# Optimization experiments

Hardware: AMD Instinct MI355X
Metric: run time of the kernel (lower is better)

The kernel has to match this reference:

```python
import jax, jax.numpy as jnp
import numpy as np
from jax import lax

B, C_IN, C_OUT, H, W = 32, 96, 96, 56, 56
E = 8          # num_experts
HID = 576      # round(96 * 6)
K = 3          # depthwise kernel size


def setup_inputs() -> dict:
    key = jax.random.key(0)
    ks = jax.random.split(key, 12)
    f = lambda k, s, sc=0.05: jax.random.normal(k, s, dtype=jnp.float32) * sc
    return {
        "x": jax.random.normal(ks[0], (B, C_IN, H, W), dtype=jnp.float32),
        # router for expand conv (input = x, C_IN channels)
        "w_r1": f(ks[1], (E, C_IN)), "b_r1": jnp.zeros((E,), jnp.float32),
        # expert bank for 1x1 expand: [E, HID, C_IN]
        "w1": f(ks[2], (E, HID, C_IN)),
        "g1": jnp.ones((HID,), jnp.float32), "bt1": jnp.zeros((HID,), jnp.float32),
        "m1": f(ks[3], (HID,), 0.01), "v1": jax.random.uniform(ks[4], (HID,), dtype=jnp.float32) + 0.5,
        # router for depthwise conv (input = expanded features, HID channels)
        "w_r2": f(ks[5], (E, HID)), "b_r2": jnp.zeros((E,), jnp.float32),
        # expert bank for depthwise 3x3: [E, HID, K, K] (in/groups = 1)
        "w2": f(ks[6], (E, HID, K, K)),
        "g2": jnp.ones((HID,), jnp.float32), "bt2": jnp.zeros((HID,), jnp.float32),
        "m2": f(ks[7], (HID,), 0.01), "v2": jax.random.uniform(ks[8], (HID,), dtype=jnp.float32) + 0.5,
        # expert bank for 1x1 project: [E, C_OUT, HID]
        "w3": f(ks[9], (E, C_OUT, HID)),
        "g3": jnp.ones((C_OUT,), jnp.float32), "bt3": jnp.zeros((C_OUT,), jnp.float32),
        "m3": f(ks[10], (C_OUT,), 0.01), "v3": jax.random.uniform(ks[11], (C_OUT,), dtype=jnp.float32) + 0.5,
        # block-level router (input = x, C_IN channels) gating the project conv
        "w_r3": f(jax.random.fold_in(key, 99), (E, C_IN)), "b_r3": jnp.zeros((E,), jnp.float32),
    }


def _route(feat, Wf, bf):
    # BasicRouter: global avg pool -> Linear -> sigmoid. feat: [B, C, H, W] -> [B, E]
    return jax.nn.sigmoid(feat.mean(axis=(2, 3)) @ Wf.T + bf)


def _bn(y, g, b, m, v, eps=1e-5):
    inv = g * lax.rsqrt(v + eps)
    return y * inv[None, :, None, None] + (b - m * inv)[None, :, None, None]


def reference(x, w_r1, b_r1, w1, g1, bt1, m1, v1,
              w_r2, b_r2, w2, g2, bt2, m2, v2,
              w3, g3, bt3, m3, v3, w_r3, b_r3):
    r1 = _route(x, w_r1, b_r1)      # [B, E] gate for expand conv
    r_blk = _route(x, w_r3, b_r3)   # [B, E] block router gates project conv

    # --- CondConv 1x1 expand: per-sample mixed kernel as batched GEMM ---
    w1c = jnp.einsum('be,eoc->boc', r1, w1)              # [B, HID, C_IN]
    y = jnp.einsum('bchw,boc->bohw', x, w1c)             # [B, HID, H, W]
    y = jnp.clip(_bn(y, g1, bt1, m1, v1), 0.0, 6.0)      # ReLU6

    # --- CondConv depthwise 3x3 (groups = HID), router on expanded feats ---
    r2 = _route(y, w_r2, b_r2)                           # [B, E]
    kw = jnp.einsum('be,eckl->bckl', r2, w2).reshape(B * HID, 1, K, K)
    y = lax.conv_general_dilated(
        y.reshape(1, B * HID, H, W), kw, (1, 1), 'SAME',
        dimension_numbers=('NCHW', 'OIHW', 'NCHW'),
        feature_group_count=B * HID).reshape(B, HID, H, W)
    y = jnp.clip(_bn(y, g2, bt2, m2, v2), 0.0, 6.0)

    # --- CondConv 1x1 project, gated by the block router(x) ---
    w3c = jnp.einsum('be,eoc->boc', r_blk, w3)           # [B, C_OUT, HID]
    y = jnp.einsum('bchw,boc->bohw', y, w3c)             # [B, C_OUT, H, W]
    y = _bn(y, g3, bt3, m3, v3)

    return x + y  # stride==1 and inp==oup -> residual connection
```

## Files before the change

### kernel.cpp

```cpp
#include <hip/hip_runtime.h>
#include <hip/hip_bf16.h>

#define B_   32
#define CIN  96
#define COUT 96
#define NP   3136
#define NE   8
#define HIDD 576

typedef short bf16x8 __attribute__((ext_vector_type(8)));
typedef float f32x4 __attribute__((ext_vector_type(4)));

__device__ __forceinline__ unsigned short f2bf(float f) {
  __hip_bfloat16 h = __float2bfloat16(f);
  unsigned short u; __builtin_memcpy(&u, &h, 2); return u;
}
__device__ __forceinline__ float bf2f(unsigned short u) {
  unsigned int v = ((unsigned int)u) << 16;
  float f; __builtin_memcpy(&f, &v, 4); return f;
}
__device__ __forceinline__ float u2f(unsigned int v) {
  float f; __builtin_memcpy(&f, &v, 4); return f;
}

__global__ __launch_bounds__(256) void k_transpose(const float* __restrict__ x,
                                                   unsigned short* __restrict__ xt,
                                                   float* __restrict__ xmean) {
  __shared__ float tile[CIN][65];
  int bi = blockIdx.x; int b = bi / 49, pt = bi % 49; int p0 = pt * 64;
  int t = threadIdx.x;
  for (int j = t; j < CIN * 64; j += 256) {
    int c = j >> 6, pi = j & 63;
    tile[c][pi] = x[((size_t)(b * CIN + c)) * NP + p0 + pi];
  }
  __syncthreads();
  if (t < CIN) {
    float s = 0.f;
    for (int i = 0; i < 64; ++i) s += tile[t][i];
    atomicAdd(xmean + b * CIN + t, s);
  }
  for (int j = t; j < 64 * CIN; j += 256) {
    int p = j / CIN, c = j % CIN;
    xt[((size_t)(b * NP + p0 + p)) * CIN + c] = f2bf(tile[c][p]);
  }
}

__global__ __launch_bounds__(64) void k_router1(const float* __restrict__ xmean,
    const float* __restrict__ wr1, const float* __restrict__ br1,
    const float* __restrict__ wr3, const float* __restrict__ br3,
    float* __restrict__ r1, float* __restrict__ rblk) {
  int bi = blockIdx.x; int lane = threadIdx.x;
  const float* wr; const float* br; float* dst; int id;
  if (bi < 256) { wr = wr1; br = br1; dst = r1;   id = bi; }
  else          { wr = wr3; br = br3; dst = rblk; id = bi - 256; }
  int b = id >> 3, e = id & 7;
  float s = 0.f;
  for (int c = lane; c < CIN; c += 64)
    s += xmean[b * CIN + c] * (1.0f / NP) * wr[e * CIN + c];
  s += __shfl_xor(s, 1);  s += __shfl_xor(s, 2);  s += __shfl_xor(s, 4);
  s += __shfl_xor(s, 8);  s += __shfl_xor(s, 16); s += __shfl_xor(s, 32);
  if (lane == 0) dst[id] = 1.0f / (1.0f + __expf(-(s + br[e])));
}

__global__ __launch_bounds__(256) void k_bnprep(
    const float* g1, const float* bt1, const float* m1, const float* v1,
    const float* g2, const float* bt2, const float* m2, const float* v2,
    const float* g3, const float* bt3, const float* m3, const float* v3,
    float* sc1, float* bi1, float* sc2, float* bi2, float* sc3, float* bi3) {
  int i = blockIdx.x * 256 + threadIdx.x;
  if (i < HIDD) {
    float s = g1[i] * rsqrtf(v1[i] + 1e-5f); sc1[i] = s; bi1[i] = bt1[i] - m1[i] * s;
  } else if (i < 2 * HIDD) {
    int c = i - HIDD;
    float s = g2[c] * rsqrtf(v2[c] + 1e-5f); sc2[c] = s; bi2[c] = bt2[c] - m2[c] * s;
  } else if (i < 2 * HIDD + COUT) {
    int c = i - 2 * HIDD;
    float s = g3[c] * rsqrtf(v3[c] + 1e-5f); sc3[c] = s; bi3[c] = bt3[c] - m3[c] * s;
  }
}

__global__ __launch_bounds__(256) void k_mixw(
    const float* __restrict__ w1, const float* __restrict__ r1, unsigned short* __restrict__ w1c,
    const float* __restrict__ w3, const float* __restrict__ rblk, unsigned short* __restrict__ w3c) {
  __shared__ float rsh[256];
  int bi = blockIdx.x; int t = threadIdx.x;
  const float* w; const float* r; unsigned short* dst; int oc0;
  if (bi < 216) { w = w1; r = r1;   dst = w1c; oc0 = bi * 256; }
  else          { w = w3; r = rblk; dst = w3c; oc0 = (bi - 216) * 256; }
  rsh[t] = r[t];
  __syncthreads();
  int oc = oc0 + t;
  float wv[NE];
#pragma unroll
  for (int e = 0; e < NE; ++e) wv[e] = w[(size_t)e * 55296 + oc];
  for (int b = 0; b < B_; ++b) {
    float a = 0.f;
#pragma unroll
    for (int e = 0; e < NE; ++e) a += rsh[b * 8 + e] * wv[e];
    dst[(size_t)b * 55296 + oc] = f2bf(a);
  }
}

__global__ __launch_bounds__(256) void k_expand2(const unsigned short* __restrict__ xt,
    const unsigned short* __restrict__ w1c, const float* __restrict__ sc1,
    const float* __restrict__ bi1, unsigned short* __restrict__ y2,
    float* __restrict__ ysum) {
  __shared__ unsigned short As[64 * 104];
  __shared__ unsigned short Bs[64 * 104];
  int t = threadIdx.x;
  int p0 = blockIdx.x * 64, o0 = blockIdx.y * 64, b = blockIdx.z;
  const unsigned short* ag = w1c + (size_t)b * 55296 + (size_t)o0 * 96;
  const unsigned short* bg = xt + ((size_t)b * NP + p0) * 96;
  for (int j = t; j < 768; j += 256) {
    int r = j / 12, ch = j % 12;
    *(int4*)(As + r * 104 + ch * 8) = *(const int4*)(ag + r * 96 + ch * 8);
    *(int4*)(Bs + r * 104 + ch * 8) = *(const int4*)(bg + r * 96 + ch * 8);
  }
  __syncthreads();
  int lane = t & 63, wv = t >> 6;
  int m = lane & 15, q = lane >> 4;
  f32x4 acc[4];
#pragma unroll
  for (int nt = 0; nt < 4; ++nt) acc[nt] = 0.f;
#pragma unroll
  for (int kk = 0; kk < 3; ++kk) {
    bf16x8 af = *(const bf16x8*)(As + (wv * 16 + m) * 104 + kk * 32 + q * 8);
#pragma unroll
    for (int nt = 0; nt < 4; ++nt) {
      bf16x8 bfb = *(const bf16x8*)(Bs + (nt * 16 + m) * 104 + kk * 32 + q * 8);
      acc[nt] = __builtin_amdgcn_mfma_f32_16x16x32_bf16(af, bfb, acc[nt], 0, 0, 0);
    }
  }
  __syncthreads();
  float sc[4], bb[4];
#pragma unroll
  for (int i = 0; i < 4; ++i) {
    int o = o0 + wv * 16 + q * 4 + i;
    sc[i] = sc1[o]; bb[i] = bi1[o];
  }
  float rs[4] = {0.f, 0.f, 0.f, 0.f};
  unsigned short* T = As;
#pragma unroll
  for (int nt = 0; nt < 4; ++nt) {
    unsigned short pk[4];
#pragma unroll
    for (int i = 0; i < 4; ++i) {
      float v = acc[nt][i] * sc[i] + bb[i];
      v = fminf(fmaxf(v, 0.f), 6.f);
      rs[i] += v;
      pk[i] = f2bf(v);
    }
    uint2 pv; __builtin_memcpy(&pv, pk, 8);
    *(uint2*)(T + (nt * 16 + m) * 72 + wv * 16 + q * 4) = pv;
  }
#pragma unroll
  for (int i = 0; i < 4; ++i) {
    float r = rs[i];
    r += __shfl_xor(r, 1); r += __shfl_xor(r, 2);
    r += __shfl_xor(r, 4); r += __shfl_xor(r, 8);
    if (m == 0) atomicAdd(ysum + b * HIDD + o0 + wv * 16 + q * 4 + i, r);
  }
  __syncthreads();
  for (int j = t; j < 512; j += 256) {
    int r = j >> 3, ch = j & 7;
    *(int4*)(y2 + ((size_t)(b * NP + p0 + r)) * 576 + o0 + ch * 8) =
        *(const int4*)(T + r * 72 + ch * 8);
  }
}

__global__ __launch_bounds__(64) void k_router2(const float* __restrict__ ysum,
    const float* __restrict__ wr2, const float* __restrict__ br2, float* __restrict__ r2) {
  int id = blockIdx.x; int lane = threadIdx.x;
  int b = id >> 3, e = id & 7;
  float s = 0.f;
  for (int h = lane; h < HIDD; h += 64)
    s += ysum[b * HIDD + h] * (1.0f / NP) * wr2[e * HIDD + h];
  s += __shfl_xor(s, 1);  s += __shfl_xor(s, 2);  s += __shfl_xor(s, 4);
  s += __shfl_xor(s, 8);  s += __shfl_xor(s, 16); s += __shfl_xor(s, 32);
  if (lane == 0) r2[id] = 1.0f / (1.0f + __expf(-(s + br2[e])));
}

__global__ __launch_bounds__(256) void k_kwmix2(const float* __restrict__ r2,
    const float* __restrict__ w2, const float* __restrict__ sc2,
    const float* __restrict__ bi2, float* __restrict__ kwt) {
  int i = blockIdx.x * 256 + threadIdx.x;
  if (i >= B_ * HIDD) return;
  int b = i / HIDD, c = i - b * HIDD;
  float rr[NE];
#pragma unroll
  for (int e = 0; e < NE; ++e) rr[e] = r2[b * 8 + e];
  float sc = sc2[c];
  float* dst = kwt + (size_t)b * 5760 + c;
#pragma unroll
  for (int k = 0; k < 9; ++k) {
    float s = 0.f;
#pragma unroll
    for (int e = 0; e < NE; ++e) s += rr[e] * w2[((size_t)e * HIDD + c) * 9 + k];
    dst[k * 576] = s * sc;
  }
  dst[9 * 576] = bi2[c];
}

__device__ __forceinline__ f32x4 cvt4(uint2 v) {
  f32x4 r;
  r[0] = u2f(v.x << 16); r[1] = u2f(v.x & 0xffff0000u);
  r[2] = u2f(v.y << 16); r[3] = u2f(v.y & 0xffff0000u);
  return r;
}
__device__ __forceinline__ uint2 pack4(f32x4 v) {
  uint2 r;
  r.x = (unsigned)f2bf(v[0]) | ((unsigned)f2bf(v[1]) << 16);
  r.y = (unsigned)f2bf(v[2]) | ((unsigned)f2bf(v[3]) << 16);
  return r;
}
__device__ __forceinline__ f32x4 clamp6(f32x4 v) {
#pragma unroll
  for (int i = 0; i < 4; ++i) v[i] = fminf(fmaxf(v[i], 0.f), 6.f);
  return v;
}

__global__ __launch_bounds__(256) void k_dwise4(const unsigned short* __restrict__ y2,
    const float* __restrict__ kwt, unsigned short* __restrict__ z2) {
  int id = blockIdx.x * 256 + threadIdx.x;
  if (id >= 28 * 144 * 32) return;
  int cg = id % 144; int rest = id / 144;
  int hp = rest % 28; int b = rest / 28;
  int c = cg * 4, h0 = hp * 2;
  const float* kp = kwt + (size_t)b * 5760 + c;
  f32x4 tk[9], tb;
#pragma unroll
  for (int k = 0; k < 9; ++k) tk[k] = *(const f32x4*)(kp + k * 576);
  tb = *(const f32x4*)(kp + 9 * 576);
  bool ok0 = (hp > 0), ok3 = (hp < 27);
  int r0 = ok0 ? (h0 - 1) : h0;
  int r3 = ok3 ? (h0 + 2) : (h0 + 1);
  const unsigned short* rowp[4];
  rowp[0] = y2 + ((size_t)(b * NP + r0 * 56)) * 576 + c;
  rowp[1] = y2 + ((size_t)(b * NP + h0 * 56)) * 576 + c;
  rowp[2] = y2 + ((size_t)(b * NP + (h0 + 1) * 56)) * 576 + c;
  rowp[3] = y2 + ((size_t)(b * NP + r3 * 56)) * 576 + c;
  bool rok[4] = {ok0, true, true, ok3};
  unsigned short* zr0 = z2 + ((size_t)(b * NP + h0 * 56)) * 576 + c;
  unsigned short* zr1 = zr0 + (size_t)56 * 576;

  f32x4 P[4], C[4], N[4];
#pragma unroll
  for (int j = 0; j < 4; ++j) P[j] = 0.f;

#define LOADCOL(D, col) do {                                           \
    _Pragma("unroll") for (int j = 0; j < 4; ++j) {                    \
      uint2 raw; raw.x = 0u; raw.y = 0u;                               \
      if ((col) < 56 && rok[j]) raw = *(const uint2*)(rowp[j] + (size_t)(col) * 576); \
      D[j] = cvt4(raw);                                                \
    } } while (0)

#define DSTEP(PP, CC, NN, wcur) do {                                   \
    f32x4 o0 = tb, o1 = tb;                                            \
    _Pragma("unroll") for (int jj = 0; jj < 3; ++jj) {                 \
      o0 += PP[jj] * tk[jj * 3] + CC[jj] * tk[jj * 3 + 1] + NN[jj] * tk[jj * 3 + 2]; \
      o1 += PP[jj + 1] * tk[jj * 3] + CC[jj + 1] * tk[jj * 3 + 1] + NN[jj + 1] * tk[jj * 3 + 2]; \
    }                                                                  \
    *(uint2*)(zr0 + (size_t)(wcur) * 576) = pack4(clamp6(o0));         \
    *(uint2*)(zr1 + (size_t)(wcur) * 576) = pack4(clamp6(o1));         \
    LOADCOL(PP, (wcur) + 2);                                           \
  } while (0)

  LOADCOL(C, 0);
  LOADCOL(N, 1);
  for (int w = 0; w < 54; w += 3) {
    DSTEP(P, C, N, w);
    DSTEP(C, N, P, w + 1);
    DSTEP(N, P, C, w + 2);
  }
  DSTEP(P, C, N, 54);
  DSTEP(C, N, P, 55);
#undef DSTEP
#undef LOADCOL
}

__global__ __launch_bounds__(384) void k_project4(const unsigned short* __restrict__ z2,
    const unsigned short* __restrict__ w3c, const float* __restrict__ sc3,
    const float* __restrict__ bi3, const float* __restrict__ x, float* __restrict__ out) {
  __shared__ unsigned short As[96 * 72];
  __shared__ unsigned short Bs[112 * 72];
  int t = threadIdx.x;
  int p0 = blockIdx.x * 112, b = blockIdx.z;
  const unsigned short* ag = w3c + (size_t)b * 55296;
  const unsigned short* zb = z2 + ((size_t)(b * NP + p0)) * 576;
  int lane = t & 63, wv = t >> 6;
  int m = lane & 15, q = lane >> 4;
  f32x4 acc[7];
#pragma unroll
  for (int nt = 0; nt < 7; ++nt) acc[nt] = 0.f;
  for (int c0 = 0; c0 < HIDD; c0 += 64) {
    __syncthreads();
    for (int j = t; j < 768; j += 384) {
      int r = j >> 3, ch = j & 7;
      *(int4*)(As + r * 72 + ch * 8) = *(const int4*)(ag + (size_t)r * 576 + c0 + ch * 8);
    }
    for (int j = t; j < 896; j += 384) {
      int r = j >> 3, ch = j & 7;
      *(int4*)(Bs + r * 72 + ch * 8) = *(const int4*)(zb + (size_t)r * 576 + c0 + ch * 8);
    }
    __syncthreads();
#pragma unroll
    for (int kk = 0; kk < 2; ++kk) {
      bf16x8 af = *(const bf16x8*)(As + (wv * 16 + m) * 72 + kk * 32 + q * 8);
#pragma unroll
      for (int nt = 0; nt < 7; ++nt) {
        bf16x8 bfb = *(const bf16x8*)(Bs + (nt * 16 + m) * 72 + kk * 32 + q * 8);
        acc[nt] = __builtin_amdgcn_mfma_f32_16x16x32_bf16(af, bfb, acc[nt], 0, 0, 0);
      }
    }
  }
#pragma unroll
  for (int i = 0; i < 4; ++i) {
    int o = wv * 16 + q * 4 + i;
    float sc = sc3[o], bb = bi3[o];
    size_t base = ((size_t)(b * COUT + o)) * NP + p0;
#pragma unroll
    for (int nt = 0; nt < 7; ++nt) {
      float v = acc[nt][i] * sc + bb + x[base + nt * 16 + m];
      out[base + nt * 16 + m] = v;
    }
  }
}

#define OFF_XT    ((size_t)0)
#define OFF_KWT   OFF_XT
#define OFF_Y     ((size_t)19267584)
#define OFF_Z     ((size_t)134873088)
#define OFF_W1C   ((size_t)250478592)
#define OFF_W3C   ((size_t)254017536)
#define OFF_XMEAN ((size_t)257556480)
#define OFF_YSUM  ((size_t)257568768)
#define OFF_R1    ((size_t)257642496)
#define OFF_RBLK  ((size_t)257643520)
#define OFF_R2    ((size_t)257644544)
#define OFF_SC1   ((size_t)257645568)
#define OFF_BI1   ((size_t)257647872)
#define OFF_SC2   ((size_t)257650176)
#define OFF_BI2   ((size_t)257652480)
#define OFF_SC3   ((size_t)257654784)
#define OFF_BI3   ((size_t)257655168)

extern "C" void kernel_launch(void* const* d_in, const int* in_sizes, int n_in,
                              void* d_out, int out_size, void* d_ws, size_t ws_size,
                              hipStream_t stream) {
  const float* x   = (const float*)d_in[0];
  const float* wr1 = (const float*)d_in[1];
  const float* br1 = (const float*)d_in[2];
  const float* w1  = (const float*)d_in[3];
  const float* g1  = (const float*)d_in[4];
  const float* bt1 = (const float*)d_in[5];
  const float* m1  = (const float*)d_in[6];
  const float* v1  = (const float*)d_in[7];
  const float* wr2 = (const float*)d_in[8];
  const float* br2 = (const float*)d_in[9];
  const float* w2  = (const float*)d_in[10];
  const float* g2  = (const float*)d_in[11];
  const float* bt2 = (const float*)d_in[12];
  const float* m2  = (const float*)d_in[13];
  const float* v2  = (const float*)d_in[14];
  const float* w3  = (const float*)d_in[15];
  const float* g3  = (const float*)d_in[16];
  const float* bt3 = (const float*)d_in[17];
  const float* m3  = (const float*)d_in[18];
  const float* v3  = (const float*)d_in[19];
  const float* wr3 = (const float*)d_in[20];
  const float* br3 = (const float*)d_in[21];
  float* out = (float*)d_out;
  char* ws = (char*)d_ws;

  unsigned short* xt   = (unsigned short*)(ws + OFF_XT);
  unsigned short* y2   = (unsigned short*)(ws + OFF_Y);
  unsigned short* z2   = (unsigned short*)(ws + OFF_Z);
  unsigned short* w1c  = (unsigned short*)(ws + OFF_W1C);
  unsigned short* w3c  = (unsigned short*)(ws + OFF_W3C);
  float* xmean = (float*)(ws + OFF_XMEAN);
  float* ysum  = (float*)(ws + OFF_YSUM);
  float* r1    = (float*)(ws + OFF_R1);
  float* rblk  = (float*)(ws + OFF_RBLK);
  float* r2    = (float*)(ws + OFF_R2);
  float* sc1   = (float*)(ws + OFF_SC1);
  float* bi1   = (float*)(ws + OFF_BI1);
  float* sc2   = (float*)(ws + OFF_SC2);
  float* bi2   = (float*)(ws + OFF_BI2);
  float* sc3   = (float*)(ws + OFF_SC3);
  float* bi3   = (float*)(ws + OFF_BI3);
  float* kwt   = (float*)(ws + OFF_KWT);

  hipMemsetAsync(ws + OFF_XMEAN, 0, 12288 + 73728, stream);

  k_transpose<<<32 * 49, 256, 0, stream>>>(x, xt, xmean);
  k_router1<<<512, 64, 0, stream>>>(xmean, wr1, br1, wr3, br3, r1, rblk);
  k_bnprep<<<5, 256, 0, stream>>>(g1, bt1, m1, v1, g2, bt2, m2, v2, g3, bt3, m3, v3,
                                  sc1, bi1, sc2, bi2, sc3, bi3);
  k_mixw<<<432, 256, 0, stream>>>(w1, r1, w1c, w3, rblk, w3c);
  k_expand2<<<dim3(49, 9, 32), 256, 0, stream>>>(xt, w1c, sc1, bi1, y2, ysum);
  k_router2<<<256, 64, 0, stream>>>(ysum, wr2, br2, r2);
  k_kwmix2<<<72, 256, 0, stream>>>(r2, w2, sc2, bi2, kwt);
  k_dwise4<<<504, 256, 0, stream>>>(y2, kwt, z2);
  k_project4<<<dim3(28, 1, 32), 384, 0, stream>>>(z2, w3c, sc3, bi3, x, out);
}
```

Measured before the change: 327.7 us.

## Widen expand tile to 192 outputs and split depthwise rows into halves

The expand GEMM kernel now computes 192 output channels per block instead of 64, so each staged pixel tile of x is reused across three times as many MFMAs and x is reloaded three times fewer. This uses more LDS per block and more accumulator registers, with launch bounds asking for three blocks per CU. The depthwise kernel now splits each row pair into two 28-column halves, doubling the thread count for more parallelism at the cost of reloading the halo columns. The bounds check is removed because 1008 blocks exactly covers the work.

```diff
diff --git a/kernel.cpp b/kernel.cpp
--- a/kernel.cpp
+++ b/kernel.cpp
@@ -101,70 +101,83 @@
   }
 }
 
-__global__ __launch_bounds__(256) void k_expand2(const unsigned short* __restrict__ xt,
+__global__ __launch_bounds__(256, 3) void k_expand3(const unsigned short* __restrict__ xt,
     const unsigned short* __restrict__ w1c, const float* __restrict__ sc1,
     const float* __restrict__ bi1, unsigned short* __restrict__ y2,
     float* __restrict__ ysum) {
-  __shared__ unsigned short As[64 * 104];
+  __shared__ unsigned short As[192 * 104];
   __shared__ unsigned short Bs[64 * 104];
   int t = threadIdx.x;
-  int p0 = blockIdx.x * 64, o0 = blockIdx.y * 64, b = blockIdx.z;
+  int p0 = blockIdx.x * 64, o0 = blockIdx.y * 192, b = blockIdx.z;
   const unsigned short* ag = w1c + (size_t)b * 55296 + (size_t)o0 * 96;
   const unsigned short* bg = xt + ((size_t)b * NP + p0) * 96;
+  for (int j = t; j < 2304; j += 256) {
+    int r = j / 12, ch = j % 12;
+    *(int4*)(As + r * 104 + ch * 8) = *(const int4*)(ag + r * 96 + ch * 8);
+  }
   for (int j = t; j < 768; j += 256) {
     int r = j / 12, ch = j % 12;
-    *(int4*)(As + r * 104 + ch * 8) = *(const int4*)(ag + r * 96 + ch * 8);
     *(int4*)(Bs + r * 104 + ch * 8) = *(const int4*)(bg + r * 96 + ch * 8);
   }
   __syncthreads();
   int lane = t & 63, wv = t >> 6;
   int m = lane & 15, q = lane >> 4;
-  f32x4 acc[4];
-#pragma unroll
-  for (int nt = 0; nt < 4; ++nt) acc[nt] = 0.f;
+  f32x4 acc[3][4];
+#pragma unroll
+  for (int ot = 0; ot < 3; ++ot)
+#pragma unroll
+    for (int nt = 0; nt < 4; ++nt) acc[ot][nt] = 0.f;
 #pragma unroll
   for (int kk = 0; kk < 3; ++kk) {
-    bf16x8 af = *(const bf16x8*)(As + (wv * 16 + m) * 104 + kk * 32 + q * 8);
+    bf16x8 af[3];
+#pragma unroll
+    for (int ot = 0; ot < 3; ++ot)
+      af[ot] = *(const bf16x8*)(As + (ot * 64 + wv * 16 + m) * 104 + kk * 32 + q * 8);
 #pragma unroll
     for (int nt = 0; nt < 4; ++nt) {
       bf16x8 bfb = *(const bf16x8*)(Bs + (nt * 16 + m) * 104 + kk * 32 + q * 8);
-      acc[nt] = __builtin_amdgcn_mfma_f32_16x16x32_bf16(af, bfb, acc[nt], 0, 0, 0);
+#pragma unroll
+      for (int ot = 0; ot < 3; ++ot)
+        acc[ot][nt] = __builtin_amdgcn_mfma_f32_16x16x32_bf16(af[ot], bfb, acc[ot][nt], 0, 0, 0);
     }
   }
   __syncthreads();
-  float sc[4], bb[4];
-#pragma unroll
-  for (int i = 0; i < 4; ++i) {
-    int o = o0 + wv * 16 + q * 4 + i;
-    sc[i] = sc1[o]; bb[i] = bi1[o];
-  }
-  float rs[4] = {0.f, 0.f, 0.f, 0.f};
   unsigned short* T = As;
 #pragma unroll
-  for (int nt = 0; nt < 4; ++nt) {
-    unsigned short pk[4];
+  for (int ot = 0; ot < 3; ++ot) {
+    float sc[4], bb[4];
 #pragma unroll
     for (int i = 0; i < 4; ++i) {
-      float v = acc[nt][i] * sc[i] + bb[i];
-      v = fminf(fmaxf(v, 0.f), 6.f);
-      rs[i] += v;
-      pk[i] = f2bf(v);
-    }
-    uint2 pv; __builtin_memcpy(&pv, pk, 8);
-    *(uint2*)(T + (nt * 16 + m) * 72 + wv * 16 + q * 4) = pv;
-  }
-#pragma unroll
-  for (int i = 0; i < 4; ++i) {
-    float r = rs[i];
-    r += __shfl_xor(r, 1); r += __shfl_xor(r, 2);
-    r += __shfl_xor(r, 4); r += __shfl_xor(r, 8);
-    if (m == 0) atomicAdd(ysum + b * HIDD + o0 + wv * 16 + q * 4 + i, r);
+      int o = o0 + ot * 64 + wv * 16 + q * 4 + i;
+      sc[i] = sc1[o]; bb[i] = bi1[o];
+    }
+    float rs[4] = {0.f, 0.f, 0.f, 0.f};
+#pragma unroll
+    for (int nt = 0; nt < 4; ++nt) {
+      unsigned short pk[4];
+#pragma unroll
+      for (int i = 0; i < 4; ++i) {
+        float v = acc[ot][nt][i] * sc[i] + bb[i];
+        v = fminf(fmaxf(v, 0.f), 6.f);
+        rs[i] += v;
+        pk[i] = f2bf(v);
+      }
+      uint2 pv; __builtin_memcpy(&pv, pk, 8);
+      *(uint2*)(T + ot * 4608 + (nt * 16 + m) * 72 + wv * 16 + q * 4) = pv;
+    }
+#pragma unroll
+    for (int i = 0; i < 4; ++i) {
+      float r = rs[i];
+      r += __shfl_xor(r, 1); r += __shfl_xor(r, 2);
+      r += __shfl_xor(r, 4); r += __shfl_xor(r, 8);
+      if (m == 0) atomicAdd(ysum + b * HIDD + o0 + ot * 64 + wv * 16 + q * 4 + i, r);
+    }
   }
   __syncthreads();
-  for (int j = t; j < 512; j += 256) {
-    int r = j >> 3, ch = j & 7;
-    *(int4*)(y2 + ((size_t)(b * NP + p0 + r)) * 576 + o0 + ch * 8) =
-        *(const int4*)(T + r * 72 + ch * 8);
+  for (int j = t; j < 1536; j += 256) {
+    int ot = j >> 9, rr = (j >> 3) & 63, ch = j & 7;
+    *(int4*)(y2 + ((size_t)(b * NP + p0 + rr)) * 576 + o0 + ot * 64 + ch * 8) =
+        *(const int4*)(T + ot * 4608 + rr * 72 + ch * 8);
   }
 }
 
@@ -219,13 +232,13 @@
   return v;
 }
 
-__global__ __launch_bounds__(256) void k_dwise4(const unsigned short* __restrict__ y2,
+__global__ __launch_bounds__(256) void k_dwise5(const unsigned short* __restrict__ y2,
     const float* __restrict__ kwt, unsigned short* __restrict__ z2) {
   int id = blockIdx.x * 256 + threadIdx.x;
-  if (id >= 28 * 144 * 32) return;
   int cg = id % 144; int rest = id / 144;
+  int wh = rest & 1; rest >>= 1;
   int hp = rest % 28; int b = rest / 28;
-  int c = cg * 4, h0 = hp * 2;
+  int c = cg * 4, h0 = hp * 2, wsrt = wh * 28;
   const float* kp = kwt + (size_t)b * 5760 + c;
   f32x4 tk[9], tb;
 #pragma unroll
@@ -244,13 +257,12 @@
   unsigned short* zr1 = zr0 + (size_t)56 * 576;
 
   f32x4 P[4], C[4], N[4];
-#pragma unroll
-  for (int j = 0; j < 4; ++j) P[j] = 0.f;
 
 #define LOADCOL(D, col) do {                                           \
     _Pragma("unroll") for (int j = 0; j < 4; ++j) {                    \
       uint2 raw; raw.x = 0u; raw.y = 0u;                               \
-      if ((col) < 56 && rok[j]) raw = *(const uint2*)(rowp[j] + (size_t)(col) * 576); \
+      if ((unsigned)(col) < 56u && rok[j])                             \
+        raw = *(const uint2*)(rowp[j] + (size_t)(col) * 576);          \
       D[j] = cvt4(raw);                                                \
     } } while (0)
 
@@ -265,15 +277,15 @@
     LOADCOL(PP, (wcur) + 2);                                           \
   } while (0)
 
-  LOADCOL(C, 0);
-  LOADCOL(N, 1);
-  for (int w = 0; w < 54; w += 3) {
+  LOADCOL(P, wsrt - 1);
+  LOADCOL(C, wsrt);
+  LOADCOL(N, wsrt + 1);
+  for (int w = wsrt; w < wsrt + 27; w += 3) {
     DSTEP(P, C, N, w);
     DSTEP(C, N, P, w + 1);
     DSTEP(N, P, C, w + 2);
   }
-  DSTEP(P, C, N, 54);
-  DSTEP(C, N, P, 55);
+  DSTEP(P, C, N, wsrt + 27);
 #undef DSTEP
 #undef LOADCOL
 }
@@ -397,9 +409,9 @@
   k_bnprep<<<5, 256, 0, stream>>>(g1, bt1, m1, v1, g2, bt2, m2, v2, g3, bt3, m3, v3,
                                   sc1, bi1, sc2, bi2, sc3, bi3);
   k_mixw<<<432, 256, 0, stream>>>(w1, r1, w1c, w3, rblk, w3c);
-  k_expand2<<<dim3(49, 9, 32), 256, 0, stream>>>(xt, w1c, sc1, bi1, y2, ysum);
+  k_expand3<<<dim3(49, 3, 32), 256, 0, stream>>>(xt, w1c, sc1, bi1, y2, ysum);
   k_router2<<<256, 64, 0, stream>>>(ysum, wr2, br2, r2);
   k_kwmix2<<<72, 256, 0, stream>>>(r2, w2, sc2, bi2, kwt);
-  k_dwise4<<<504, 256, 0, stream>>>(y2, kwt, z2);
+  k_dwise5<<<1008, 256, 0, stream>>>(y2, kwt, z2);
   k_project4<<<dim3(28, 1, 32), 384, 0, stream>>>(z2, w3c, sc3, bi3, x, out);
 }
```

Result: no change. 332.3 us (+1.4%).

## Replace atomic reductions with partial sums, merge small kernels, split depthwise width

Applied to the files above, without the earlier changes.

Global-mean reductions for the routers now write per-tile partial sums instead of doing atomicAdd. The small kernels are fused: router1 with BN prep, and router2 with kernel-weight mixing. That removes the memset and two launches. The depthwise kernel now splits each row pair into two 28-column halves, doubling the grid to 1008 blocks for more parallelism, at the cost of loading one extra halo column per half. Partial-sum buffers reuse the z2 workspace region, which is safe because z2 is written only after they are consumed.

```diff
diff --git a/kernel.cpp b/kernel.cpp
--- a/kernel.cpp
+++ b/kernel.cpp
@@ -25,7 +25,7 @@
 
 __global__ __launch_bounds__(256) void k_transpose(const float* __restrict__ x,
                                                    unsigned short* __restrict__ xt,
-                                                   float* __restrict__ xmean) {
+                                                   float* __restrict__ xpart) {
   __shared__ float tile[CIN][65];
   int bi = blockIdx.x; int b = bi / 49, pt = bi % 49; int p0 = pt * 64;
   int t = threadIdx.x;
@@ -37,7 +37,7 @@
   if (t < CIN) {
     float s = 0.f;
     for (int i = 0; i < 64; ++i) s += tile[t][i];
-    atomicAdd(xmean + b * CIN + t, s);
+    xpart[((size_t)(b * 49 + pt)) * CIN + t] = s;
   }
   for (int j = t; j < 64 * CIN; j += 256) {
     int p = j / CIN, c = j % CIN;
@@ -45,37 +45,42 @@
   }
 }
 
-__global__ __launch_bounds__(64) void k_router1(const float* __restrict__ xmean,
+__global__ __launch_bounds__(64) void k_front(const float* __restrict__ xpart,
     const float* __restrict__ wr1, const float* __restrict__ br1,
     const float* __restrict__ wr3, const float* __restrict__ br3,
-    float* __restrict__ r1, float* __restrict__ rblk) {
-  int bi = blockIdx.x; int lane = threadIdx.x;
-  const float* wr; const float* br; float* dst; int id;
-  if (bi < 256) { wr = wr1; br = br1; dst = r1;   id = bi; }
-  else          { wr = wr3; br = br3; dst = rblk; id = bi - 256; }
-  int b = id >> 3, e = id & 7;
-  float s = 0.f;
-  for (int c = lane; c < CIN; c += 64)
-    s += xmean[b * CIN + c] * (1.0f / NP) * wr[e * CIN + c];
-  s += __shfl_xor(s, 1);  s += __shfl_xor(s, 2);  s += __shfl_xor(s, 4);
-  s += __shfl_xor(s, 8);  s += __shfl_xor(s, 16); s += __shfl_xor(s, 32);
-  if (lane == 0) dst[id] = 1.0f / (1.0f + __expf(-(s + br[e])));
-}
-
-__global__ __launch_bounds__(256) void k_bnprep(
+    float* __restrict__ r1, float* __restrict__ rblk,
     const float* g1, const float* bt1, const float* m1, const float* v1,
     const float* g2, const float* bt2, const float* m2, const float* v2,
     const float* g3, const float* bt3, const float* m3, const float* v3,
     float* sc1, float* bi1, float* sc2, float* bi2, float* sc3, float* bi3) {
-  int i = blockIdx.x * 256 + threadIdx.x;
-  if (i < HIDD) {
-    float s = g1[i] * rsqrtf(v1[i] + 1e-5f); sc1[i] = s; bi1[i] = bt1[i] - m1[i] * s;
-  } else if (i < 2 * HIDD) {
-    int c = i - HIDD;
-    float s = g2[c] * rsqrtf(v2[c] + 1e-5f); sc2[c] = s; bi2[c] = bt2[c] - m2[c] * s;
-  } else if (i < 2 * HIDD + COUT) {
-    int c = i - 2 * HIDD;
-    float s = g3[c] * rsqrtf(v3[c] + 1e-5f); sc3[c] = s; bi3[c] = bt3[c] - m3[c] * s;
+  int bi = blockIdx.x; int lane = threadIdx.x;
+  if (bi < 512) {
+    const float* wr; const float* br; float* dst; int id;
+    if (bi < 256) { wr = wr1; br = br1; dst = r1;   id = bi; }
+    else          { wr = wr3; br = br3; dst = rblk; id = bi - 256; }
+    int b = id >> 3, e = id & 7;
+    float s = 0.f;
+    for (int c = lane; c < CIN; c += 64) {
+      const float* xp = xpart + (size_t)b * 49 * CIN + c;
+      float xm = 0.f;
+#pragma unroll 7
+      for (int k = 0; k < 49; ++k) xm += xp[k * CIN];
+      s += xm * (1.0f / NP) * wr[e * CIN + c];
+    }
+    s += __shfl_xor(s, 1);  s += __shfl_xor(s, 2);  s += __shfl_xor(s, 4);
+    s += __shfl_xor(s, 8);  s += __shfl_xor(s, 16); s += __shfl_xor(s, 32);
+    if (lane == 0) dst[id] = 1.0f / (1.0f + __expf(-(s + br[e])));
+  } else {
+    int i = (bi - 512) * 64 + lane;
+    if (i < HIDD) {
+      float s = g1[i] * rsqrtf(v1[i] + 1e-5f); sc1[i] = s; bi1[i] = bt1[i] - m1[i] * s;
+    } else if (i < 2 * HIDD) {
+      int c = i - HIDD;
+      float s = g2[c] * rsqrtf(v2[c] + 1e-5f); sc2[c] = s; bi2[c] = bt2[c] - m2[c] * s;
+    } else if (i < 2 * HIDD + COUT) {
+      int c = i - 2 * HIDD;
+      float s = g3[c] * rsqrtf(v3[c] + 1e-5f); sc3[c] = s; bi3[c] = bt3[c] - m3[c] * s;
+    }
   }
 }
 
@@ -104,11 +109,12 @@
 __global__ __launch_bounds__(256) void k_expand2(const unsigned short* __restrict__ xt,
     const unsigned short* __restrict__ w1c, const float* __restrict__ sc1,
     const float* __restrict__ bi1, unsigned short* __restrict__ y2,
-    float* __restrict__ ysum) {
+    float* __restrict__ yspart) {
   __shared__ unsigned short As[64 * 104];
   __shared__ unsigned short Bs[64 * 104];
   int t = threadIdx.x;
-  int p0 = blockIdx.x * 64, o0 = blockIdx.y * 64, b = blockIdx.z;
+  int pt = blockIdx.x;
+  int p0 = pt * 64, o0 = blockIdx.y * 64, b = blockIdx.z;
   const unsigned short* ag = w1c + (size_t)b * 55296 + (size_t)o0 * 96;
   const unsigned short* bg = xt + ((size_t)b * NP + p0) * 96;
   for (int j = t; j < 768; j += 256) {
@@ -158,7 +164,8 @@
     float r = rs[i];
     r += __shfl_xor(r, 1); r += __shfl_xor(r, 2);
     r += __shfl_xor(r, 4); r += __shfl_xor(r, 8);
-    if (m == 0) atomicAdd(ysum + b * HIDD + o0 + wv * 16 + q * 4 + i, r);
+    if (m == 0)
+      yspart[((size_t)b * 49 + pt) * HIDD + o0 + wv * 16 + q * 4 + i] = r;
   }
   __syncthreads();
   for (int j = t; j < 512; j += 256) {
@@ -168,37 +175,46 @@
   }
 }
 
-__global__ __launch_bounds__(64) void k_router2(const float* __restrict__ ysum,
-    const float* __restrict__ wr2, const float* __restrict__ br2, float* __restrict__ r2) {
-  int id = blockIdx.x; int lane = threadIdx.x;
-  int b = id >> 3, e = id & 7;
-  float s = 0.f;
-  for (int h = lane; h < HIDD; h += 64)
-    s += ysum[b * HIDD + h] * (1.0f / NP) * wr2[e * HIDD + h];
-  s += __shfl_xor(s, 1);  s += __shfl_xor(s, 2);  s += __shfl_xor(s, 4);
-  s += __shfl_xor(s, 8);  s += __shfl_xor(s, 16); s += __shfl_xor(s, 32);
-  if (lane == 0) r2[id] = 1.0f / (1.0f + __expf(-(s + br2[e])));
-}
-
-__global__ __launch_bounds__(256) void k_kwmix2(const float* __restrict__ r2,
+__global__ __launch_bounds__(256) void k_mid(const float* __restrict__ yspart,
+    const float* __restrict__ wr2, const float* __restrict__ br2,
     const float* __restrict__ w2, const float* __restrict__ sc2,
     const float* __restrict__ bi2, float* __restrict__ kwt) {
-  int i = blockIdx.x * 256 + threadIdx.x;
-  if (i >= B_ * HIDD) return;
-  int b = i / HIDD, c = i - b * HIDD;
+  __shared__ float ysum_l[HIDD];
+  __shared__ float r2_l[NE];
+  int b = blockIdx.x, t = threadIdx.x;
+  const float* yp = yspart + (size_t)b * 49 * HIDD;
+  for (int c = t; c < HIDD; c += 256) {
+    float s = 0.f;
+#pragma unroll 7
+    for (int k = 0; k < 49; ++k) s += yp[k * HIDD + c];
+    ysum_l[c] = s;
+  }
+  __syncthreads();
+  int wv = t >> 6, lane = t & 63;
+  for (int e = wv; e < NE; e += 4) {
+    float s = 0.f;
+    for (int h = lane; h < HIDD; h += 64)
+      s += ysum_l[h] * (1.0f / NP) * wr2[e * HIDD + h];
+    s += __shfl_xor(s, 1);  s += __shfl_xor(s, 2);  s += __shfl_xor(s, 4);
+    s += __shfl_xor(s, 8);  s += __shfl_xor(s, 16); s += __shfl_xor(s, 32);
+    if (lane == 0) r2_l[e] = 1.0f / (1.0f + __expf(-(s + br2[e])));
+  }
+  __syncthreads();
   float rr[NE];
 #pragma unroll
-  for (int e = 0; e < NE; ++e) rr[e] = r2[b * 8 + e];
-  float sc = sc2[c];
-  float* dst = kwt + (size_t)b * 5760 + c;
-#pragma unroll
-  for (int k = 0; k < 9; ++k) {
-    float s = 0.f;
-#pragma unroll
-    for (int e = 0; e < NE; ++e) s += rr[e] * w2[((size_t)e * HIDD + c) * 9 + k];
-    dst[k * 576] = s * sc;
-  }
-  dst[9 * 576] = bi2[c];
+  for (int e = 0; e < NE; ++e) rr[e] = r2_l[e];
+  for (int c = t; c < HIDD; c += 256) {
+    float sc = sc2[c];
+    float* dst = kwt + (size_t)b * 5760 + c;
+#pragma unroll
+    for (int k = 0; k < 9; ++k) {
+      float s = 0.f;
+#pragma unroll
+      for (int e = 0; e < NE; ++e) s += rr[e] * w2[((size_t)e * HIDD + c) * 9 + k];
+      dst[k * 576] = s * sc;
+    }
+    dst[9 * 576] = bi2[c];
+  }
 }
 
 __device__ __forceinline__ f32x4 cvt4(uint2 v) {
@@ -219,13 +235,13 @@
   return v;
 }
 
-__global__ __launch_bounds__(256) void k_dwise4(const unsigned short* __restrict__ y2,
+__global__ __launch_bounds__(256) void k_dwise5(const unsigned short* __restrict__ y2,
     const float* __restrict__ kwt, unsigned short* __restrict__ z2) {
   int id = blockIdx.x * 256 + threadIdx.x;
-  if (id >= 28 * 144 * 32) return;
   int cg = id % 144; int rest = id / 144;
+  int wh = rest & 1; rest >>= 1;
   int hp = rest % 28; int b = rest / 28;
-  int c = cg * 4, h0 = hp * 2;
+  int c = cg * 4, h0 = hp * 2, wsrt = wh * 28;
   const float* kp = kwt + (size_t)b * 5760 + c;
   f32x4 tk[9], tb;
 #pragma unroll
@@ -244,13 +260,12 @@
   unsigned short* zr1 = zr0 + (size_t)56 * 576;
 
   f32x4 P[4], C[4], N[4];
-#pragma unroll
-  for (int j = 0; j < 4; ++j) P[j] = 0.f;
 
 #define LOADCOL(D, col) do {                                           \
     _Pragma("unroll") for (int j = 0; j < 4; ++j) {                    \
       uint2 raw; raw.x = 0u; raw.y = 0u;                               \
-      if ((col) < 56 && rok[j]) raw = *(const uint2*)(rowp[j] + (size_t)(col) * 576); \
+      if ((unsigned)(col) < 56u && rok[j])                             \
+        raw = *(const uint2*)(rowp[j] + (size_t)(col) * 576);          \
       D[j] = cvt4(raw);                                                \
     } } while (0)
 
@@ -265,15 +280,15 @@
     LOADCOL(PP, (wcur) + 2);                                           \
   } while (0)
 
-  LOADCOL(C, 0);
-  LOADCOL(N, 1);
-  for (int w = 0; w < 54; w += 3) {
+  LOADCOL(P, wsrt - 1);
+  LOADCOL(C, wsrt);
+  LOADCOL(N, wsrt + 1);
+  for (int w = wsrt; w < wsrt + 27; w += 3) {
     DSTEP(P, C, N, w);
     DSTEP(C, N, P, w + 1);
     DSTEP(N, P, C, w + 2);
   }
-  DSTEP(P, C, N, 54);
-  DSTEP(C, N, P, 55);
+  DSTEP(P, C, N, wsrt + 27);
 #undef DSTEP
 #undef LOADCOL
 }
@@ -326,23 +341,22 @@
   }
 }
 
-#define OFF_XT    ((size_t)0)
-#define OFF_KWT   OFF_XT
-#define OFF_Y     ((size_t)19267584)
-#define OFF_Z     ((size_t)134873088)
-#define OFF_W1C   ((size_t)250478592)
-#define OFF_W3C   ((size_t)254017536)
-#define OFF_XMEAN ((size_t)257556480)
-#define OFF_YSUM  ((size_t)257568768)
-#define OFF_R1    ((size_t)257642496)
-#define OFF_RBLK  ((size_t)257643520)
-#define OFF_R2    ((size_t)257644544)
-#define OFF_SC1   ((size_t)257645568)
-#define OFF_BI1   ((size_t)257647872)
-#define OFF_SC2   ((size_t)257650176)
-#define OFF_BI2   ((size_t)257652480)
-#define OFF_SC3   ((size_t)257654784)
-#define OFF_BI3   ((size_t)257655168)
+#define OFF_XT     ((size_t)0)
+#define OFF_KWT    OFF_XT
+#define OFF_Y      ((size_t)19267584)
+#define OFF_Z      ((size_t)134873088)
+#define OFF_XPART  OFF_Z
+#define OFF_YSPART (OFF_Z + 602112)
+#define OFF_W1C    ((size_t)250478592)
+#define OFF_W3C    ((size_t)254017536)
+#define OFF_R1     ((size_t)257642496)
+#define OFF_RBLK   ((size_t)257643520)
+#define OFF_SC1    ((size_t)257645568)
+#define OFF_BI1    ((size_t)257647872)
+#define OFF_SC2    ((size_t)257650176)
+#define OFF_BI2    ((size_t)257652480)
+#define OFF_SC3    ((size_t)257654784)
+#define OFF_BI3    ((size_t)257655168)
 
 extern "C" void kernel_launch(void* const* d_in, const int* in_sizes, int n_in,
                               void* d_out, int out_size, void* d_ws, size_t ws_size,
@@ -372,34 +386,30 @@
   float* out = (float*)d_out;
   char* ws = (char*)d_ws;
 
-  unsigned short* xt   = (unsigned short*)(ws + OFF_XT);
-  unsigned short* y2   = (unsigned short*)(ws + OFF_Y);
-  unsigned short* z2   = (unsigned short*)(ws + OFF_Z);
-  unsigned short* w1c  = (unsigned short*)(ws + OFF_W1C);
-  unsigned short* w3c  = (unsigned short*)(ws + OFF_W3C);
-  float* xmean = (float*)(ws + OFF_XMEAN);
-  float* ysum  = (float*)(ws + OFF_YSUM);
-  float* r1    = (float*)(ws + OFF_R1);
-  float* rblk  = (float*)(ws + OFF_RBLK);
-  float* r2    = (float*)(ws + OFF_R2);
-  float* sc1   = (float*)(ws + OFF_SC1);
-  float* bi1   = (float*)(ws + OFF_BI1);
-  float* sc2   = (float*)(ws + OFF_SC2);
-  float* bi2   = (float*)(ws + OFF_BI2);
-  float* sc3   = (float*)(ws + OFF_SC3);
-  float* bi3   = (float*)(ws + OFF_BI3);
-  float* kwt   = (float*)(ws + OFF_KWT);
-
-  hipMemsetAsync(ws + OFF_XMEAN, 0, 12288 + 73728, stream);
-
-  k_transpose<<<32 * 49, 256, 0, stream>>>(x, xt, xmean);
-  k_router1<<<512, 64, 0, stream>>>(xmean, wr1, br1, wr3, br3, r1, rblk);
-  k_bnprep<<<5, 256, 0, stream>>>(g1, bt1, m1, v1, g2, bt2, m2, v2, g3, bt3, m3, v3,
+  unsigned short* xt     = (unsigned short*)(ws + OFF_XT);
+  unsigned short* y2     = (unsigned short*)(ws + OFF_Y);
+  unsigned short* z2     = (unsigned short*)(ws + OFF_Z);
+  unsigned short* w1c    = (unsigned short*)(ws + OFF_W1C);
+  unsigned short* w3c    = (unsigned short*)(ws + OFF_W3C);
+  float* xpart  = (float*)(ws + OFF_XPART);
+  float* yspart = (float*)(ws + OFF_YSPART);
+  float* r1     = (float*)(ws + OFF_R1);
+  float* rblk   = (float*)(ws + OFF_RBLK);
+  float* sc1    = (float*)(ws + OFF_SC1);
+  float* bi1    = (float*)(ws + OFF_BI1);
+  float* sc2    = (float*)(ws + OFF_SC2);
+  float* bi2    = (float*)(ws + OFF_BI2);
+  float* sc3    = (float*)(ws + OFF_SC3);
+  float* bi3    = (float*)(ws + OFF_BI3);
+  float* kwt    = (float*)(ws + OFF_KWT);
+
+  k_transpose<<<32 * 49, 256, 0, stream>>>(x, xt, xpart);
+  k_front<<<532, 64, 0, stream>>>(xpart, wr1, br1, wr3, br3, r1, rblk,
+                                  g1, bt1, m1, v1, g2, bt2, m2, v2, g3, bt3, m3, v3,
                                   sc1, bi1, sc2, bi2, sc3, bi3);
   k_mixw<<<432, 256, 0, stream>>>(w1, r1, w1c, w3, rblk, w3c);
-  k_expand2<<<dim3(49, 9, 32), 256, 0, stream>>>(xt, w1c, sc1, bi1, y2, ysum);
-  k_router2<<<256, 64, 0, stream>>>(ysum, wr2, br2, r2);
-  k_kwmix2<<<72, 256, 0, stream>>>(r2, w2, sc2, bi2, kwt);
-  k_dwise4<<<504, 256, 0, stream>>>(y2, kwt, z2);
+  k_expand2<<<dim3(49, 9, 32), 256, 0, stream>>>(xt, w1c, sc1, bi1, y2, yspart);
+  k_mid<<<32, 256, 0, stream>>>(yspart, wr2, br2, w2, sc2, bi2, kwt);
+  k_dwise5<<<1008, 256, 0, stream>>>(y2, kwt, z2);
   k_project4<<<dim3(28, 1, 32), 384, 0, stream>>>(z2, w3c, sc3, bi3, x, out);
 }
```

Measured after the change: 321.9 us. No clear change (-1.8%).
